# Kernel tuning notes

Measured on AMD Instinct MI355X. Metric: run time of the kernel, lower is better.

## Reference

```python
import jax, jax.numpy as jnp
import numpy as np
from jax import lax

N, D, M, H = 8192, 32, 8, 128
ATOL = 1e-5
RTOL = 1e-5
MAX_STEPS = 10   # bounded adaptive dopri5 iterations (accept/reject with masking)
DT0 = 0.25


def setup_inputs() -> dict:
    key = jax.random.key(0)
    ks = jax.random.split(key, 6)
    p = lambda k, shape, s: jax.random.normal(k, shape, jnp.float32) * s
    return {
        "z": jax.random.normal(ks[0], (N, D), jnp.float32),
        "G_w": p(ks[1], (M, D), 0.3),
        "W1": p(ks[2], (H, D), (1.0 / D) ** 0.5),
        "b1": jnp.zeros((H,), jnp.float32),
        "W2": p(ks[3], (H, H), (1.0 / H) ** 0.5),
        "b2": jnp.zeros((H,), jnp.float32),
        "W3": p(ks[4], (D, H), (1.0 / H) ** 0.5),
        "b3": jnp.zeros((D,), jnp.float32),
        "T": jnp.ones((1,), jnp.float32),
    }


def qpnf_forward(z, G_w, W1, b1, W2, b2, W3, b3, T):
    d = z.shape[1]

    def mlp(x):  # dF network: d -> 128 -> 128 -> d
        h = jax.nn.relu(x @ W1.T + b1)
        h = jax.nn.relu(h @ W2.T + b2)
        return h @ W3.T + b3

    # G is linear (no bias) so jacrev(G)(x) == G_w for every sample; the batched
    # dG @ dG^T solves collapse to one shared (m,m) solve / (d,d) projector.
    A = G_w @ G_w.T                       # (m, m)
    AinvG = jnp.linalg.solve(A, G_w)      # (m, d) = A^{-1} W
    P = G_w.T @ AinvG                     # (d, d) null-space projector W^T A^{-1} W
    IP = jnp.eye(d, dtype=z.dtype) - P
    trP = jnp.trace(P)

    jac_mlp = jax.vmap(jax.jacrev(lambda xi: mlp(xi[None, :])[0]))  # (N,d,d)

    def f(y):  # augmented state y = [x | logp], dlogp/dt = -div(dx/dx)
        x = y[:, :d]
        dF = mlp(x)                        # (N, d)
        g = x @ G_w.T                      # (N, m)
        dz = -(dF @ IP) - g @ AinvG        # -(eta_J) - (eta_C)
        JdF = jac_mlp(x)                   # (N, d, d)
        # J_f = -(I-P) JdF - P  ->  dlogp = -trace(J_f)
        dlogp = jnp.einsum('jk,nkj->n', IP, JdF) + trP
        return jnp.concatenate([dz, dlogp[:, None]], axis=1)

    def rk_step(y, dt):  # Dormand-Prince 5(4)
        k1 = f(y)
        k2 = f(y + dt * (0.2 * k1))
        k3 = f(y + dt * (3/40 * k1 + 9/40 * k2))
        k4 = f(y + dt * (44/45 * k1 - 56/15 * k2 + 32/9 * k3))
        k5 = f(y + dt * (19372/6561 * k1 - 25360/2187 * k2 + 64448/6561 * k3 - 212/729 * k4))
        k6 = f(y + dt * (9017/3168 * k1 - 355/33 * k2 + 46732/5247 * k3 + 49/176 * k4 - 5103/18656 * k5))
        y1 = y + dt * (35/384 * k1 + 500/1113 * k3 + 125/192 * k4 - 2187/6784 * k5 + 11/84 * k6)
        k7 = f(y1)
        err = dt * ((35/384 - 5179/57600) * k1 + (500/1113 - 7571/16695) * k3
                    + (125/192 - 393/640) * k4 + (-2187/6784 + 92097/339200) * k5
                    + (11/84 - 187/2100) * k6 - (1/40) * k7)
        return y1, err

    t1 = 2.0 * T[0]  # eval path: integration_times[-1] *= 2
    y0 = jnp.concatenate([z, jnp.zeros((z.shape[0], 1), z.dtype)], axis=1)

    def body(carry, _):
        t, dt, y = carry
        done = t >= t1 - 1e-9
        dtc = jnp.where(done, jnp.asarray(1e-3, z.dtype), jnp.minimum(dt, t1 - t))
        y1, ev = rk_step(y, dtc)
        tol = ATOL + RTOL * jnp.maximum(jnp.abs(y), jnp.abs(y1))
        errn = jnp.sqrt(jnp.mean((ev / tol) ** 2))
        accept = jnp.logical_and(~done, errn <= 1.0)
        y_new = jnp.where(accept, y1, y)
        t_new = jnp.where(accept, t + dtc, t)
        factor = jnp.clip(0.9 * errn ** (-0.2), 0.2, 10.0)
        dt_new = jnp.where(done, dt, jnp.clip(dtc * factor, 1e-6, t1))
        dt_new = lax.stop_gradient(dt_new)
        return (t_new, dt_new, y_new), None

    init = (jnp.asarray(0.0, z.dtype), jnp.asarray(DT0, z.dtype), y0)
    (_, _, yT), _ = lax.scan(body, init, None, length=MAX_STEPS)
    return yT[:, :d]


def reference(z, G_w, W1, b1, W2, b2, W3, b3, T):
    return qpnf_forward(z, G_w, W1, b1, W2, b2, W3, b3, T)
```

## Files before the change

### kernel.cpp

```cpp
#include <hip/hip_runtime.h>
#include <hip/hip_cooperative_groups.h>
#include <math.h>

namespace cg = cooperative_groups;
typedef float4 f4;

#define NT 512
#define RB 32

#define WS_WR    0
#define WS_PART  32768
#define WS_TOTAL 35328

#define L_W1T   0
#define L_C3T   4096
#define L_P     8320
#define L_PT    9344
#define L_HST   10496
#define L_HS2   15104
#define L_XST   19712
#define L_B1    20864
#define L_B2    20992
#define L_C0    21120
#define L_GS    21152
#define L_AAUG  21408
#define L_AINVG 21536
#define L_MISC  21792
#define L_KZ    21796
#define L_KL    29860
#define L_YZ    30084
#define L_Y1Z   31236
#define L_YL    32388
#define L_Y1L   32420
#define LDS_FLOATS 32452
#define L_RED   L_XST

__device__ const float ACO[5][5] = {
  { 0.2f, 0.f, 0.f, 0.f, 0.f },
  { (float)(3.0/40.0), (float)(9.0/40.0), 0.f, 0.f, 0.f },
  { (float)(44.0/45.0), (float)(-56.0/15.0), (float)(32.0/9.0), 0.f, 0.f },
  { (float)(19372.0/6561.0), (float)(-25360.0/2187.0), (float)(64448.0/6561.0), (float)(-212.0/729.0), 0.f },
  { (float)(9017.0/3168.0), (float)(-355.0/33.0), (float)(46732.0/5247.0), (float)(49.0/176.0), (float)(-5103.0/18656.0) }
};

#define B1C ((float)(35.0/384.0))
#define B3C ((float)(500.0/1113.0))
#define B4C ((float)(125.0/192.0))
#define B5C ((float)(-2187.0/6784.0))
#define B6C ((float)(11.0/84.0))

#define E1C ((float)(35.0/384.0 - 5179.0/57600.0))
#define E3C ((float)(500.0/1113.0 - 7571.0/16695.0))
#define E4C ((float)(125.0/192.0 - 393.0/640.0))
#define E5C ((float)(-2187.0/6784.0 + 92097.0/339200.0))
#define E6C ((float)(11.0/84.0 - 187.0/2100.0))
#define E7C ((float)(-1.0/40.0))

__device__ __forceinline__ f4 ld4(const float* p){ return *(const f4*)p; }
__device__ __forceinline__ void st4(float* p, f4 v){ *(f4*)p = v; }

__device__ void assemble_x(float* lds, int tid, float dtc, const float* co, int np)
{
  __syncthreads();
  if (tid < 256){
    const int r = tid >> 3, jj = (tid & 7) * 4;
    const int o = r * 36 + jj;
    f4 y = ld4(&lds[L_YZ + o]);
    float sx = 0.f, sy = 0.f, sz = 0.f, sw = 0.f;
    for (int p = 0; p < np; p++){
      f4 kv = ld4(&lds[L_KZ + p * 1152 + o]);
      float c = co[p];
      sx += c * kv.x; sy += c * kv.y; sz += c * kv.z; sw += c * kv.w;
    }
    lds[L_XST + (jj + 0) * 36 + r] = y.x + dtc * sx;
    lds[L_XST + (jj + 1) * 36 + r] = y.y + dtc * sy;
    lds[L_XST + (jj + 2) * 36 + r] = y.z + dtc * sz;
    lds[L_XST + (jj + 3) * 36 + r] = y.w + dtc * sw;
  }
  __syncthreads();
}

__device__ void eval_f(float* lds, const float* __restrict__ ws, int tid,
                       float trP, int kout)
{
  const int cg = tid & 31, kh = (tid >> 5) & 1, wv = tid >> 6;
  const int row4 = 4 * wv;

  float a1[4][4];
#pragma unroll
  for (int i = 0; i < 4; i++)
#pragma unroll
    for (int j = 0; j < 4; j++) a1[i][j] = 0.f;
#pragma unroll 4
  for (int t = 0; t < 16; t++){
    const int k = kh * 16 + t;
    f4 av = ld4(&lds[L_XST + k * 36 + row4]);
    f4 bv = ld4(&lds[L_W1T + k * 128 + 4 * cg]);
    const float* ap = (const float*)&av;
    const float* bp = (const float*)&bv;
#pragma unroll
    for (int i = 0; i < 4; i++)
#pragma unroll
      for (int j = 0; j < 4; j++) a1[i][j] += bp[i] * ap[j];
  }
#pragma unroll
  for (int i = 0; i < 4; i++)
#pragma unroll
    for (int j = 0; j < 4; j++) a1[i][j] += __shfl_xor(a1[i][j], 32);
  if (kh == 0){
    f4 b1v = ld4(&lds[L_B1 + 4 * cg]);
    const float* b1p = (const float*)&b1v;
#pragma unroll
    for (int i = 0; i < 4; i++){
      f4 hv; float* hp = (float*)&hv;
#pragma unroll
      for (int j = 0; j < 4; j++) hp[j] = fmaxf(a1[i][j] + b1p[i], 0.f);
      st4(&lds[L_HST + (4 * cg + i) * 36 + row4], hv);
    }
  }
  __syncthreads();

  float ah[4][4], at[4][4];
#pragma unroll
  for (int i = 0; i < 4; i++)
#pragma unroll
    for (int j = 0; j < 4; j++){ ah[i][j] = 0.f; at[i][j] = 0.f; }
  const f4* WR4 = (const f4*)&ws[WS_WR];
  const int kb = kh * 64;
  f4 wb[4], rb[4];
#pragma unroll
  for (int u = 0; u < 4; u++){
    wb[u] = WR4[(kb + u) * 64 + cg];
    rb[u] = WR4[(kb + u) * 64 + 32 + cg];
  }
#pragma unroll 1
  for (int g = 0; g < 16; g++){
    f4 wc[4], rc[4];
#pragma unroll
    for (int u = 0; u < 4; u++){ wc[u] = wb[u]; rc[u] = rb[u]; }
    if (g < 15){
      const int kn = kb + (g + 1) * 4;
#pragma unroll
      for (int u = 0; u < 4; u++){
        wb[u] = WR4[(kn + u) * 64 + cg];
        rb[u] = WR4[(kn + u) * 64 + 32 + cg];
      }
    }
#pragma unroll
    for (int u = 0; u < 4; u++){
      const int k = kb + g * 4 + u;
      f4 av = ld4(&lds[L_HST + k * 36 + row4]);
      const float* ap = (const float*)&av;
      const float* wp = (const float*)&wc[u];
      const float* rp = (const float*)&rc[u];
      float m[4];
#pragma unroll
      for (int j = 0; j < 4; j++) m[j] = (ap[j] > 0.f) ? 1.f : 0.f;
#pragma unroll
      for (int i = 0; i < 4; i++)
#pragma unroll
        for (int j = 0; j < 4; j++){
          ah[i][j] += wp[i] * ap[j];
          at[i][j] += rp[i] * m[j];
        }
    }
  }
#pragma unroll
  for (int i = 0; i < 4; i++)
#pragma unroll
    for (int j = 0; j < 4; j++){
      ah[i][j] += __shfl_xor(ah[i][j], 32);
      at[i][j] += __shfl_xor(at[i][j], 32);
    }

  f4 b2v = ld4(&lds[L_B2 + 4 * cg]);
  const float* b2p = (const float*)&b2v;
  float h2v[4][4]; float dl[4] = {0.f, 0.f, 0.f, 0.f};
#pragma unroll
  for (int i = 0; i < 4; i++)
#pragma unroll
    for (int j = 0; j < 4; j++){
      float pre = ah[i][j] + b2p[i];
      float hv = fmaxf(pre, 0.f);
      h2v[i][j] = hv;
      if (pre > 0.f) dl[j] += at[i][j];
    }
#pragma unroll
  for (int mk = 1; mk < 32; mk <<= 1){
#pragma unroll
    for (int j = 0; j < 4; j++) dl[j] += __shfl_xor(dl[j], mk, 64);
  }
  if (kh == 0){
#pragma unroll
    for (int i = 0; i < 4; i++){
      f4 hv; float* hp = (float*)&hv;
#pragma unroll
      for (int j = 0; j < 4; j++) hp[j] = h2v[i][j];
      st4(&lds[L_HS2 + (4 * cg + i) * 36 + row4], hv);
    }
    if (cg == 0){
#pragma unroll
      for (int j = 0; j < 4; j++)
        lds[L_KL + kout * 32 + row4 + j] = dl[j] + trP;
    }
  }
  __syncthreads();

  float a3[4] = {0.f, 0.f, 0.f, 0.f};
  const int bb = kh * 64;
#pragma unroll 4
  for (int t = 0; t < 16; t++){
    f4 cv = ld4(&lds[L_C3T + cg * 132 + bb + 4 * t]);
    const float* cp = (const float*)&cv;
#pragma unroll
    for (int u = 0; u < 4; u++){
      f4 av = ld4(&lds[L_HS2 + (bb + 4 * t + u) * 36 + row4]);
      const float* ap = (const float*)&av;
#pragma unroll
      for (int j = 0; j < 4; j++) a3[j] += ap[j] * cp[u];
    }
  }
  const int qq = kh * 16;
#pragma unroll
  for (int t = 0; t < 4; t++){
    f4 pv = ld4(&lds[L_PT + cg * 36 + qq + 4 * t]);
    const float* pp = (const float*)&pv;
#pragma unroll
    for (int u = 0; u < 4; u++){
      f4 av = ld4(&lds[L_XST + (qq + 4 * t + u) * 36 + row4]);
      const float* ap = (const float*)&av;
#pragma unroll
      for (int j = 0; j < 4; j++) a3[j] += ap[j] * pp[u];
    }
  }
#pragma unroll
  for (int j = 0; j < 4; j++) a3[j] += __shfl_xor(a3[j], 32);
  if (kh == 0){
    float c0v = lds[L_C0 + cg];
#pragma unroll
    for (int j = 0; j < 4; j++)
      lds[L_KZ + kout * 1152 + (row4 + j) * 36 + cg] = -(a3[j] + c0v);
  }
}

__global__ void __launch_bounds__(NT, 2)
qpnf_kernel(const float* __restrict__ z, const float* __restrict__ Gw,
            const float* __restrict__ W1g, const float* __restrict__ b1g,
            const float* __restrict__ W2g, const float* __restrict__ b2g,
            const float* __restrict__ W3g, const float* __restrict__ b3g,
            const float* __restrict__ Tg, float* __restrict__ out,
            float* __restrict__ ws)
{
  __shared__ float lds[LDS_FLOATS];
  const int tid = threadIdx.x;
  const int bid = blockIdx.x;
  const int r0 = bid * RB;
  cg::grid_group grid = cg::this_grid();

  for (int i = 0; i < 8; i++){
    int idx = tid + i * NT;
    int h = idx >> 5, j = idx & 31;
    lds[L_W1T + j * 128 + h] = W1g[idx];
  }
  if (tid < 128){ lds[L_B1 + tid] = b1g[tid]; lds[L_B2 + tid] = b2g[tid]; }
  if (tid < 256) lds[L_GS + tid] = Gw[tid];
  __syncthreads();

  if (tid < 64){
    int i = tid >> 3, j = tid & 7;
    float s = 0.f;
    for (int k = 0; k < 32; k++) s += lds[L_GS + i * 32 + k] * lds[L_GS + j * 32 + k];
    lds[L_AAUG + i * 16 + j] = s;
    lds[L_AAUG + i * 16 + 8 + j] = (i == j) ? 1.f : 0.f;
  }
  __syncthreads();
  if (tid == 0){
    float* A = &lds[L_AAUG];
    for (int c = 0; c < 8; c++){
      int p = c; float mx = fabsf(A[c * 16 + c]);
      for (int r = c + 1; r < 8; r++){
        float v = fabsf(A[r * 16 + c]);
        if (v > mx){ mx = v; p = r; }
      }
      if (p != c)
        for (int q = 0; q < 16; q++){ float t = A[c*16+q]; A[c*16+q] = A[p*16+q]; A[p*16+q] = t; }
      float pv = 1.0f / A[c * 16 + c];
      for (int q = 0; q < 16; q++) A[c * 16 + q] *= pv;
      for (int r = 0; r < 8; r++) if (r != c){
        float fct = A[r * 16 + c];
        for (int q = 0; q < 16; q++) A[r * 16 + q] -= fct * A[c * 16 + q];
      }
    }
  }
  __syncthreads();
  if (tid < 256){
    int m = tid >> 5, d = tid & 31;
    float s = 0.f;
    for (int q = 0; q < 8; q++) s += lds[L_AAUG + m * 16 + 8 + q] * lds[L_GS + q * 32 + d];
    lds[L_AINVG + m * 32 + d] = s;
  }
  __syncthreads();
  for (int i4 = 0; i4 < 2; i4++){
    int idx = tid + i4 * NT;
    int i = idx >> 5, j = idx & 31;
    float s = 0.f;
    for (int m = 0; m < 8; m++) s += lds[L_GS + m * 32 + i] * lds[L_AINVG + m * 32 + j];
    lds[L_P + i * 32 + j] = s;
  }
  __syncthreads();
  float* IPl = &lds[L_XST];
  for (int i4 = 0; i4 < 2; i4++){
    int idx = tid + i4 * NT;
    int i = idx >> 5, j = idx & 31;
    IPl[i * 32 + j] = ((i == j) ? 1.f : 0.f) - lds[L_P + i * 32 + j];
  }
  if (tid == 0){
    float s = 0.f;
    for (int i = 0; i < 32; i++) s += lds[L_P + i * 32 + i];
    lds[L_MISC] = s;
  }
  __syncthreads();
  for (int i4 = 0; i4 < 8; i4++){
    int idx = tid + i4 * NT;
    int b = idx & 127, c = idx >> 7;
    float s = 0.f;
    for (int i = 0; i < 32; i++) s += W3g[i * 128 + b] * IPl[i * 32 + c];
    lds[L_C3T + c * 132 + b] = s;
  }
  for (int i4 = 0; i4 < 2; i4++){
    int idx = tid + i4 * NT;
    int c = idx >> 5, q = idx & 31;
    lds[L_PT + c * 36 + q] = lds[L_P + q * 32 + c];
  }
  if (tid < 32){
    float s = 0.f;
    for (int i = 0; i < 32; i++) s += b3g[i] * IPl[i * 32 + tid];
    lds[L_C0 + tid] = s;
  }
  for (int i4 = 0; i4 < 8; i4++){
    int idx = tid + i4 * NT;
    int j = idx >> 7, b = idx & 127;
    float s = 0.f;
    for (int k = 0; k < 32; k++) s += IPl[j * 32 + k] * W3g[k * 128 + b];
    lds[L_HST + j * 128 + b] = s;
  }
  __syncthreads();
  if (bid < 128 && tid < 128){
    int a = bid;
    float s = 0.f;
    for (int j = 0; j < 32; j++) s += W1g[a * 32 + j] * lds[L_HST + j * 128 + tid];
    ws[WS_WR + a * 256 + 128 + tid] = s * W2g[tid * 128 + a];
  }
  if (bid >= 128 && tid < 128){
    int a = bid - 128;
    ws[WS_WR + a * 256 + tid] = W2g[tid * 128 + a];
  }
  if (tid < 256){
    const int r = tid >> 3, jj = (tid & 7) * 4;
    st4(&lds[L_YZ + r * 36 + jj], ld4(&z[(r0 + r) * 32 + jj]));
  }
  if (tid < RB) lds[L_YL + tid] = 0.f;

  const float trP = lds[L_MISC];
  const float t1 = 2.0f * Tg[0];

  grid.sync();

  float t_cur = 0.f, dt_cur = 0.25f;
  bool prev_acc = false;

  for (int step = 0; step < 10; step++){
    if (t_cur >= t1 - 1e-9f) break;
    const float dtc = fminf(dt_cur, t1 - t_cur);

    for (int s = 1; s <= 6; s++){
      if (s == 1 && step > 0){
        if (prev_acc){
          if (tid < 256){
            const int r = tid >> 3, jj = (tid & 7) * 4;
            const int o = r * 36 + jj;
            st4(&lds[L_KZ + o], ld4(&lds[L_KZ + 6 * 1152 + o]));
          }
          if (tid < RB) lds[L_KL + tid] = lds[L_KL + 6 * 32 + tid];
        }
        continue;
      }
      assemble_x(lds, tid, dtc, ACO[s >= 2 ? s - 2 : 0], s - 1);
      eval_f(lds, ws, tid, trP, s - 1);
    }

    __syncthreads();
    if (tid < 256){
      const int r = tid >> 3, jj = (tid & 7) * 4;
      const int o = r * 36 + jj;
      f4 y   = ld4(&lds[L_YZ + o]);
      f4 k1v = ld4(&lds[L_KZ + 0 * 1152 + o]);
      f4 k3v = ld4(&lds[L_KZ + 2 * 1152 + o]);
      f4 k4v = ld4(&lds[L_KZ + 3 * 1152 + o]);
      f4 k5v = ld4(&lds[L_KZ + 4 * 1152 + o]);
      f4 k6v = ld4(&lds[L_KZ + 5 * 1152 + o]);
      f4 x;
      x.x = y.x + dtc * (B1C*k1v.x + B3C*k3v.x + B4C*k4v.x + B5C*k5v.x + B6C*k6v.x);
      x.y = y.y + dtc * (B1C*k1v.y + B3C*k3v.y + B4C*k4v.y + B5C*k5v.y + B6C*k6v.y);
      x.z = y.z + dtc * (B1C*k1v.z + B3C*k3v.z + B4C*k4v.z + B5C*k5v.z + B6C*k6v.z);
      x.w = y.w + dtc * (B1C*k1v.w + B3C*k3v.w + B4C*k4v.w + B5C*k5v.w + B6C*k6v.w);
      st4(&lds[L_Y1Z + o], x);
      lds[L_XST + (jj + 0) * 36 + r] = x.x;
      lds[L_XST + (jj + 1) * 36 + r] = x.y;
      lds[L_XST + (jj + 2) * 36 + r] = x.z;
      lds[L_XST + (jj + 3) * 36 + r] = x.w;
    }
    if (tid < RB){
      float s = B1C * lds[L_KL + 0*32 + tid] + B3C * lds[L_KL + 2*32 + tid]
              + B4C * lds[L_KL + 3*32 + tid] + B5C * lds[L_KL + 4*32 + tid]
              + B6C * lds[L_KL + 5*32 + tid];
      lds[L_Y1L + tid] = lds[L_YL + tid] + dtc * s;
    }
    __syncthreads();
    eval_f(lds, ws, tid, trP, 6);
    __syncthreads();

    float sacc = 0.f;
    if (tid < 256){
      const int r = tid >> 3, jj = (tid & 7) * 4;
      const int o = r * 36 + jj;
      f4 k1v = ld4(&lds[L_KZ + 0 * 1152 + o]);
      f4 k3v = ld4(&lds[L_KZ + 2 * 1152 + o]);
      f4 k4v = ld4(&lds[L_KZ + 3 * 1152 + o]);
      f4 k5v = ld4(&lds[L_KZ + 4 * 1152 + o]);
      f4 k6v = ld4(&lds[L_KZ + 5 * 1152 + o]);
      f4 k7v = ld4(&lds[L_KZ + 6 * 1152 + o]);
      f4 yv  = ld4(&lds[L_YZ + o]);
      f4 y1v = ld4(&lds[L_Y1Z + o]);
      float ev, tol, q;
      ev = dtc * (E1C*k1v.x + E3C*k3v.x + E4C*k4v.x + E5C*k5v.x + E6C*k6v.x + E7C*k7v.x);
      tol = 1e-5f + 1e-5f * fmaxf(fabsf(yv.x), fabsf(y1v.x)); q = ev / tol; sacc += q * q;
      ev = dtc * (E1C*k1v.y + E3C*k3v.y + E4C*k4v.y + E5C*k5v.y + E6C*k6v.y + E7C*k7v.y);
      tol = 1e-5f + 1e-5f * fmaxf(fabsf(yv.y), fabsf(y1v.y)); q = ev / tol; sacc += q * q;
      ev = dtc * (E1C*k1v.z + E3C*k3v.z + E4C*k4v.z + E5C*k5v.z + E6C*k6v.z + E7C*k7v.z);
      tol = 1e-5f + 1e-5f * fmaxf(fabsf(yv.z), fabsf(y1v.z)); q = ev / tol; sacc += q * q;
      ev = dtc * (E1C*k1v.w + E3C*k3v.w + E4C*k4v.w + E5C*k5v.w + E6C*k6v.w + E7C*k7v.w);
      tol = 1e-5f + 1e-5f * fmaxf(fabsf(yv.w), fabsf(y1v.w)); q = ev / tol; sacc += q * q;
    }
    if (tid < RB){
      float evl = dtc * (E1C * lds[L_KL + 0*32 + tid] + E3C * lds[L_KL + 2*32 + tid]
                + E4C * lds[L_KL + 3*32 + tid] + E5C * lds[L_KL + 4*32 + tid]
                + E6C * lds[L_KL + 5*32 + tid] + E7C * lds[L_KL + 6*32 + tid]);
      float toll = 1e-5f + 1e-5f * fmaxf(fabsf(lds[L_YL + tid]), fabsf(lds[L_Y1L + tid]));
      float ql = evl / toll; sacc += ql * ql;
    }
    __syncthreads();
    lds[L_RED + tid] = sacc; __syncthreads();
    for (int o = 256; o > 0; o >>= 1){
      if (tid < o) lds[L_RED + tid] += lds[L_RED + tid + o];
      __syncthreads();
    }
    if (tid == 0) ws[WS_PART + step * 256 + bid] = lds[L_RED + 0];

    grid.sync();

    if (tid < 256) lds[L_RED + tid] = ws[WS_PART + step * 256 + tid];
    __syncthreads();
    for (int o = 128; o > 0; o >>= 1){
      if (tid < o) lds[L_RED + tid] += lds[L_RED + tid + o];
      __syncthreads();
    }
    const float errn = sqrtf(lds[L_RED + 0] / 270336.0f);
    __syncthreads();

    const bool accept = (errn <= 1.0f);
    if (accept){
      if (tid < 256){
        const int r = tid >> 3, jj = (tid & 7) * 4;
        const int o = r * 36 + jj;
        st4(&lds[L_YZ + o], ld4(&lds[L_Y1Z + o]));
      }
      if (tid < RB) lds[L_YL + tid] = lds[L_Y1L + tid];
      t_cur += dtc;
    }
    float fac = 0.9f * powf(errn, -0.2f);
    fac = fminf(fmaxf(fac, 0.2f), 10.0f);
    dt_cur = fminf(fmaxf(dtc * fac, 1e-6f), t1);
    prev_acc = accept;
  }

  __syncthreads();
  if (tid < 256){
    const int r = tid >> 3, jj = (tid & 7) * 4;
    st4(&out[(r0 + r) * 32 + jj], ld4(&lds[L_YZ + r * 36 + jj]));
  }
}

extern "C" void kernel_launch(void* const* d_in, const int* in_sizes, int n_in,
                              void* d_out, int out_size, void* d_ws, size_t ws_size,
                              hipStream_t stream)
{
  (void)in_sizes; (void)n_in; (void)out_size;
  const float* z  = (const float*)d_in[0];
  const float* Gw = (const float*)d_in[1];
  const float* W1 = (const float*)d_in[2];
  const float* b1 = (const float*)d_in[3];
  const float* W2 = (const float*)d_in[4];
  const float* b2 = (const float*)d_in[5];
  const float* W3 = (const float*)d_in[6];
  const float* b3 = (const float*)d_in[7];
  const float* T  = (const float*)d_in[8];
  float* out = (float*)d_out;
  float* ws  = (float*)d_ws;
  if (ws_size < (size_t)WS_TOTAL * sizeof(float)) return;

  void* args[] = { (void*)&z, (void*)&Gw, (void*)&W1, (void*)&b1, (void*)&W2,
                   (void*)&b2, (void*)&W3, (void*)&b3, (void*)&T, (void*)&out,
                   (void*)&ws };
  hipLaunchCooperativeKernel((const void*)qpnf_kernel, dim3(256), dim3(NT),
                             args, 0, stream);
}
```

Before: 1.300 ms.

## Give each wave its own rows so RK stage evaluation avoids block barriers

Each wave now owns 4 rows of the block's 32-row tile and runs the MLP stage evaluation on private per-wave LDS buffers with swizzled layouts. This replaces the block-wide __syncthreads between stages with wave-local fences, and the final error reduction uses wave shuffles instead of a shared-memory tree. The cost is that each wave now reads all of W2/W3 (global WR loads and LDS C3T) for only 4 rows, which raises weight traffic per row. Correctness relies on wave-lockstep execution with only __threadfence_block for ordering.

```diff
diff --git a/kernel.cpp b/kernel.cpp
--- a/kernel.cpp
+++ b/kernel.cpp
@@ -4,6 +4,7 @@
 
 namespace cg = cooperative_groups;
 typedef float4 f4;
+typedef float2 f2;
 
 #define NT 512
 #define RB 32
@@ -13,27 +14,31 @@
 #define WS_TOTAL 35328
 
 #define L_W1T   0
-#define L_C3T   4096
-#define L_P     8320
-#define L_PT    9344
-#define L_HST   10496
-#define L_HS2   15104
-#define L_XST   19712
-#define L_B1    20864
-#define L_B2    20992
-#define L_C0    21120
-#define L_GS    21152
-#define L_AAUG  21408
-#define L_AINVG 21536
-#define L_MISC  21792
-#define L_KZ    21796
-#define L_KL    29860
-#define L_YZ    30084
-#define L_Y1Z   31236
-#define L_YL    32388
-#define L_Y1L   32420
-#define LDS_FLOATS 32452
-#define L_RED   L_XST
+#define L_C3T   4240
+#define L_PT    8976
+#define L_KZ    10384
+#define L_KL    18448
+#define L_YZ    18672
+#define L_Y1Z   19824
+#define L_YL    20976
+#define L_Y1L   21008
+#define L_B1    21040
+#define L_B2    21168
+#define L_C0    21296
+#define L_MISC  21328
+#define L_RED8  21332
+#define L_WV    21340
+#define WVSZ    1200
+#define WV_XW   0
+#define WV_HW   140
+#define WV_H2   668
+#define LDS_FLOATS 30940
+
+#define LI_GS    (L_WV + 0)
+#define LI_AAUG  (L_WV + 256)
+#define LI_AINVG (L_WV + 384)
+#define LI_P     (L_WV + 640)
+#define LI_IPW3  (L_WV + 1664)
 
 __device__ const float ACO[5][5] = {
   { 0.2f, 0.f, 0.f, 0.f, 0.f },
@@ -59,188 +64,235 @@
 __device__ __forceinline__ f4 ld4(const float* p){ return *(const f4*)p; }
 __device__ __forceinline__ void st4(float* p, f4 v){ *(f4*)p = v; }
 
-__device__ void assemble_x(float* lds, int tid, float dtc, const float* co, int np)
+__device__ void assemble_wave(float* lds, int lane, int w, float dtc,
+                              const float* co, int np)
 {
-  __syncthreads();
-  if (tid < 256){
-    const int r = tid >> 3, jj = (tid & 7) * 4;
-    const int o = r * 36 + jj;
-    f4 y = ld4(&lds[L_YZ + o]);
-    float sx = 0.f, sy = 0.f, sz = 0.f, sw = 0.f;
-    for (int p = 0; p < np; p++){
-      f4 kv = ld4(&lds[L_KZ + p * 1152 + o]);
-      float c = co[p];
-      sx += c * kv.x; sy += c * kv.y; sz += c * kv.z; sw += c * kv.w;
-    }
-    lds[L_XST + (jj + 0) * 36 + r] = y.x + dtc * sx;
-    lds[L_XST + (jj + 1) * 36 + r] = y.y + dtc * sy;
-    lds[L_XST + (jj + 2) * 36 + r] = y.z + dtc * sz;
-    lds[L_XST + (jj + 3) * 36 + r] = y.w + dtc * sw;
-  }
-  __syncthreads();
+  const int row = lane >> 4, c0 = 2 * (lane & 15);
+  const int yo = (4 * w + row) * 36 + c0;
+  f2 y = *(const f2*)&lds[L_YZ + yo];
+  float sx = 0.f, sy = 0.f;
+  for (int p = 0; p < np; p++){
+    f2 kv = *(const f2*)&lds[L_KZ + p * 1152 + yo];
+    sx += co[p] * kv.x; sy += co[p] * kv.y;
+  }
+  float* XW = &lds[L_WV + w * WVSZ + WV_XW];
+  const int s0 = 4 * c0 + 4 * ((c0 >> 3) & 3);
+  XW[s0 + row]     = y.x + dtc * sx;
+  XW[s0 + 4 + row] = y.y + dtc * sy;
+  __threadfence_block();
 }
 
-__device__ void eval_f(float* lds, const float* __restrict__ ws, int tid,
-                       float trP, int kout)
+__device__ void eval_wave(float* lds, const float* __restrict__ ws,
+                          int lane, int w, float trP, int kout)
 {
-  const int cg = tid & 31, kh = (tid >> 5) & 1, wv = tid >> 6;
-  const int row4 = 4 * wv;
-
-  float a1[4][4];
-#pragma unroll
-  for (int i = 0; i < 4; i++)
+  const int cg = lane & 15, kh = lane >> 4;
+  float* XW = &lds[L_WV + w * WVSZ + WV_XW];
+  float* HW = &lds[L_WV + w * WVSZ + WV_HW];
+  float* H2 = &lds[L_WV + w * WVSZ + WV_H2];
+
+  float a1[8][4];
+#pragma unroll
+  for (int i = 0; i < 8; i++)
 #pragma unroll
     for (int j = 0; j < 4; j++) a1[i][j] = 0.f;
-#pragma unroll 4
-  for (int t = 0; t < 16; t++){
-    const int k = kh * 16 + t;
-    f4 av = ld4(&lds[L_XST + k * 36 + row4]);
-    f4 bv = ld4(&lds[L_W1T + k * 128 + 4 * cg]);
+#pragma unroll
+  for (int t = 0; t < 8; t++){
+    const int k = kh * 8 + t;
+    f4 av = ld4(&XW[4 * k + 4 * kh]);
+    f4 b0 = ld4(&lds[L_W1T + k * 132 + 4 * kh + 8 * cg]);
+    f4 b1v = ld4(&lds[L_W1T + k * 132 + 4 * kh + 8 * cg + 4]);
     const float* ap = (const float*)&av;
-    const float* bp = (const float*)&bv;
+    const float* bp0 = (const float*)&b0;
+    const float* bp1 = (const float*)&b1v;
 #pragma unroll
     for (int i = 0; i < 4; i++)
 #pragma unroll
-      for (int j = 0; j < 4; j++) a1[i][j] += bp[i] * ap[j];
-  }
-#pragma unroll
-  for (int i = 0; i < 4; i++)
-#pragma unroll
-    for (int j = 0; j < 4; j++) a1[i][j] += __shfl_xor(a1[i][j], 32);
+      for (int j = 0; j < 4; j++){
+        a1[i][j]     += bp0[i] * ap[j];
+        a1[4 + i][j] += bp1[i] * ap[j];
+      }
+  }
+#pragma unroll
+  for (int i = 0; i < 8; i++)
+#pragma unroll
+    for (int j = 0; j < 4; j++){
+      a1[i][j] += __shfl_xor(a1[i][j], 16);
+      a1[i][j] += __shfl_xor(a1[i][j], 32);
+    }
   if (kh == 0){
-    f4 b1v = ld4(&lds[L_B1 + 4 * cg]);
-    const float* b1p = (const float*)&b1v;
-#pragma unroll
-    for (int i = 0; i < 4; i++){
+    f4 bb0 = ld4(&lds[L_B1 + 8 * cg]);
+    f4 bb1 = ld4(&lds[L_B1 + 8 * cg + 4]);
+    const float* bp0 = (const float*)&bb0;
+    const float* bp1 = (const float*)&bb1;
+    const int swz = 4 * ((cg >> 2) & 3);
+#pragma unroll
+    for (int i = 0; i < 8; i++){
+      float bi = (i < 4) ? bp0[i] : bp1[i - 4];
       f4 hv; float* hp = (float*)&hv;
 #pragma unroll
-      for (int j = 0; j < 4; j++) hp[j] = fmaxf(a1[i][j] + b1p[i], 0.f);
-      st4(&lds[L_HST + (4 * cg + i) * 36 + row4], hv);
-    }
-  }
-  __syncthreads();
-
-  float ah[4][4], at[4][4];
-#pragma unroll
-  for (int i = 0; i < 4; i++)
+      for (int j = 0; j < 4; j++) hp[j] = fmaxf(a1[i][j] + bi, 0.f);
+      st4(&HW[4 * (8 * cg + i) + swz], hv);
+    }
+  }
+  __threadfence_block();
+
+  float ah[8][4], at[8][4];
+#pragma unroll
+  for (int i = 0; i < 8; i++)
 #pragma unroll
     for (int j = 0; j < 4; j++){ ah[i][j] = 0.f; at[i][j] = 0.f; }
   const f4* WR4 = (const f4*)&ws[WS_WR];
-  const int kb = kh * 64;
-  f4 wb[4], rb[4];
-#pragma unroll
-  for (int u = 0; u < 4; u++){
-    wb[u] = WR4[(kb + u) * 64 + cg];
-    rb[u] = WR4[(kb + u) * 64 + 32 + cg];
+  const int kb = kh * 32;
+  f4 buf[8];
+#pragma unroll
+  for (int e = 0; e < 2; e++){
+    buf[4*e+0] = WR4[(kb + e) * 64 + 2 * cg];
+    buf[4*e+1] = WR4[(kb + e) * 64 + 2 * cg + 1];
+    buf[4*e+2] = WR4[(kb + e) * 64 + 32 + 2 * cg];
+    buf[4*e+3] = WR4[(kb + e) * 64 + 32 + 2 * cg + 1];
   }
 #pragma unroll 1
   for (int g = 0; g < 16; g++){
-    f4 wc[4], rc[4];
-#pragma unroll
-    for (int u = 0; u < 4; u++){ wc[u] = wb[u]; rc[u] = rb[u]; }
+    f4 cur[8];
+#pragma unroll
+    for (int u = 0; u < 8; u++) cur[u] = buf[u];
     if (g < 15){
-      const int kn = kb + (g + 1) * 4;
-#pragma unroll
-      for (int u = 0; u < 4; u++){
-        wb[u] = WR4[(kn + u) * 64 + cg];
-        rb[u] = WR4[(kn + u) * 64 + 32 + cg];
-      }
-    }
+      const int kn = kb + 2 * (g + 1);
+#pragma unroll
+      for (int e = 0; e < 2; e++){
+        buf[4*e+0] = WR4[(kn + e) * 64 + 2 * cg];
+        buf[4*e+1] = WR4[(kn + e) * 64 + 2 * cg + 1];
+        buf[4*e+2] = WR4[(kn + e) * 64 + 32 + 2 * cg];
+        buf[4*e+3] = WR4[(kn + e) * 64 + 32 + 2 * cg + 1];
+      }
+    }
+#pragma unroll
+    for (int e = 0; e < 2; e++){
+      const int k = kb + 2 * g + e;
+      f4 av = ld4(&HW[4 * k + 4 * kh]);
+      const float* ap = (const float*)&av;
+      const float* wa = (const float*)&cur[4*e+0];
+      const float* wb = (const float*)&cur[4*e+1];
+      const float* ra = (const float*)&cur[4*e+2];
+      const float* rb = (const float*)&cur[4*e+3];
+      float m[4];
+#pragma unroll
+      for (int j = 0; j < 4; j++) m[j] = (ap[j] > 0.f) ? 1.f : 0.f;
+#pragma unroll
+      for (int i = 0; i < 4; i++)
+#pragma unroll
+        for (int j = 0; j < 4; j++){
+          ah[i][j]     += wa[i] * ap[j];
+          ah[4 + i][j] += wb[i] * ap[j];
+          at[i][j]     += ra[i] * m[j];
+          at[4 + i][j] += rb[i] * m[j];
+        }
+    }
+  }
+#pragma unroll
+  for (int i = 0; i < 8; i++)
+#pragma unroll
+    for (int j = 0; j < 4; j++){
+      ah[i][j] += __shfl_xor(ah[i][j], 16);
+      ah[i][j] += __shfl_xor(ah[i][j], 32);
+      at[i][j] += __shfl_xor(at[i][j], 16);
+      at[i][j] += __shfl_xor(at[i][j], 32);
+    }
+
+  f4 b2a = ld4(&lds[L_B2 + 8 * cg]);
+  f4 b2b = ld4(&lds[L_B2 + 8 * cg + 4]);
+  const float* b2p0 = (const float*)&b2a;
+  const float* b2p1 = (const float*)&b2b;
+  float h2v[8][4]; float dl[4] = {0.f, 0.f, 0.f, 0.f};
+#pragma unroll
+  for (int i = 0; i < 8; i++){
+    float bi = (i < 4) ? b2p0[i] : b2p1[i - 4];
+#pragma unroll
+    for (int j = 0; j < 4; j++){
+      float pre = ah[i][j] + bi;
+      h2v[i][j] = fmaxf(pre, 0.f);
+      if (pre > 0.f) dl[j] += at[i][j];
+    }
+  }
+#pragma unroll
+  for (int mk = 1; mk < 16; mk <<= 1){
+#pragma unroll
+    for (int j = 0; j < 4; j++) dl[j] += __shfl_xor(dl[j], mk);
+  }
+  if (lane == 0){
+#pragma unroll
+    for (int j = 0; j < 4; j++)
+      lds[L_KL + kout * 32 + 4 * w + j] = dl[j] + trP;
+  }
+  if (kh == 0){
+    const int swz = 4 * ((cg >> 2) & 3);
+#pragma unroll
+    for (int i = 0; i < 8; i++){
+      f4 hv; float* hp = (float*)&hv;
+#pragma unroll
+      for (int j = 0; j < 4; j++) hp[j] = h2v[i][j];
+      st4(&H2[4 * (8 * cg + i) + swz], hv);
+    }
+  }
+  __threadfence_block();
+
+  float a3[2][4] = {{0.f,0.f,0.f,0.f},{0.f,0.f,0.f,0.f}};
+  const int cc0 = 2 * cg, cc1 = 2 * cg + 1;
+  const int bb = kh * 32;
+#pragma unroll 2
+  for (int t = 0; t < 8; t++){
+    const int b4 = bb + 4 * t;
+    f4 cva = ld4(&lds[L_C3T + cc0 * 148 + b4 + 4 * kh]);
+    f4 cvb = ld4(&lds[L_C3T + cc1 * 148 + b4 + 4 * kh]);
+    const float* ca = (const float*)&cva;
+    const float* cb = (const float*)&cvb;
 #pragma unroll
     for (int u = 0; u < 4; u++){
-      const int k = kb + g * 4 + u;
-      f4 av = ld4(&lds[L_HST + k * 36 + row4]);
+      f4 av = ld4(&H2[4 * (b4 + u) + 4 * kh]);
       const float* ap = (const float*)&av;
-      const float* wp = (const float*)&wc[u];
-      const float* rp = (const float*)&rc[u];
-      float m[4];
-#pragma unroll
-      for (int j = 0; j < 4; j++) m[j] = (ap[j] > 0.f) ? 1.f : 0.f;
-#pragma unroll
-      for (int i = 0; i < 4; i++)
-#pragma unroll
-        for (int j = 0; j < 4; j++){
-          ah[i][j] += wp[i] * ap[j];
-          at[i][j] += rp[i] * m[j];
-        }
-    }
-  }
-#pragma unroll
-  for (int i = 0; i < 4; i++)
+#pragma unroll
+      for (int j = 0; j < 4; j++){
+        a3[0][j] += ap[j] * ca[u];
+        a3[1][j] += ap[j] * cb[u];
+      }
+    }
+  }
+  const int qq = kh * 8;
+#pragma unroll
+  for (int t = 0; t < 2; t++){
+    const int q4 = qq + 4 * t;
+    f4 pva = ld4(&lds[L_PT + cc0 * 44 + q4 + 4 * kh]);
+    f4 pvb = ld4(&lds[L_PT + cc1 * 44 + q4 + 4 * kh]);
+    const float* pa = (const float*)&pva;
+    const float* pb = (const float*)&pvb;
+#pragma unroll
+    for (int u = 0; u < 4; u++){
+      f4 av = ld4(&XW[4 * (q4 + u) + 4 * kh]);
+      const float* ap = (const float*)&av;
+#pragma unroll
+      for (int j = 0; j < 4; j++){
+        a3[0][j] += ap[j] * pa[u];
+        a3[1][j] += ap[j] * pb[u];
+      }
+    }
+  }
+#pragma unroll
+  for (int j = 0; j < 4; j++){
+    a3[0][j] += __shfl_xor(a3[0][j], 16);
+    a3[0][j] += __shfl_xor(a3[0][j], 32);
+    a3[1][j] += __shfl_xor(a3[1][j], 16);
+    a3[1][j] += __shfl_xor(a3[1][j], 32);
+  }
+  if (kh == 0){
+    float c0v = lds[L_C0 + cc0];
+    float c1v = lds[L_C0 + cc1];
 #pragma unroll
     for (int j = 0; j < 4; j++){
-      ah[i][j] += __shfl_xor(ah[i][j], 32);
-      at[i][j] += __shfl_xor(at[i][j], 32);
-    }
-
-  f4 b2v = ld4(&lds[L_B2 + 4 * cg]);
-  const float* b2p = (const float*)&b2v;
-  float h2v[4][4]; float dl[4] = {0.f, 0.f, 0.f, 0.f};
-#pragma unroll
-  for (int i = 0; i < 4; i++)
-#pragma unroll
-    for (int j = 0; j < 4; j++){
-      float pre = ah[i][j] + b2p[i];
-      float hv = fmaxf(pre, 0.f);
-      h2v[i][j] = hv;
-      if (pre > 0.f) dl[j] += at[i][j];
-    }
-#pragma unroll
-  for (int mk = 1; mk < 32; mk <<= 1){
-#pragma unroll
-    for (int j = 0; j < 4; j++) dl[j] += __shfl_xor(dl[j], mk, 64);
-  }
-  if (kh == 0){
-#pragma unroll
-    for (int i = 0; i < 4; i++){
-      f4 hv; float* hp = (float*)&hv;
-#pragma unroll
-      for (int j = 0; j < 4; j++) hp[j] = h2v[i][j];
-      st4(&lds[L_HS2 + (4 * cg + i) * 36 + row4], hv);
-    }
-    if (cg == 0){
-#pragma unroll
-      for (int j = 0; j < 4; j++)
-        lds[L_KL + kout * 32 + row4 + j] = dl[j] + trP;
-    }
-  }
-  __syncthreads();
-
-  float a3[4] = {0.f, 0.f, 0.f, 0.f};
-  const int bb = kh * 64;
-#pragma unroll 4
-  for (int t = 0; t < 16; t++){
-    f4 cv = ld4(&lds[L_C3T + cg * 132 + bb + 4 * t]);
-    const float* cp = (const float*)&cv;
-#pragma unroll
-    for (int u = 0; u < 4; u++){
-      f4 av = ld4(&lds[L_HS2 + (bb + 4 * t + u) * 36 + row4]);
-      const float* ap = (const float*)&av;
-#pragma unroll
-      for (int j = 0; j < 4; j++) a3[j] += ap[j] * cp[u];
-    }
-  }
-  const int qq = kh * 16;
-#pragma unroll
-  for (int t = 0; t < 4; t++){
-    f4 pv = ld4(&lds[L_PT + cg * 36 + qq + 4 * t]);
-    const float* pp = (const float*)&pv;
-#pragma unroll
-    for (int u = 0; u < 4; u++){
-      f4 av = ld4(&lds[L_XST + (qq + 4 * t + u) * 36 + row4]);
-      const float* ap = (const float*)&av;
-#pragma unroll
-      for (int j = 0; j < 4; j++) a3[j] += ap[j] * pp[u];
-    }
-  }
-#pragma unroll
-  for (int j = 0; j < 4; j++) a3[j] += __shfl_xor(a3[j], 32);
-  if (kh == 0){
-    float c0v = lds[L_C0 + cg];
-#pragma unroll
-    for (int j = 0; j < 4; j++)
-      lds[L_KZ + kout * 1152 + (row4 + j) * 36 + cg] = -(a3[j] + c0v);
-  }
+      f2 kv; kv.x = -(a3[0][j] + c0v); kv.y = -(a3[1][j] + c1v);
+      *(f2*)&lds[L_KZ + kout * 1152 + (4 * w + j) * 36 + cc0] = kv;
+    }
+  }
+  __threadfence_block();
 }
 
 __global__ void __launch_bounds__(NT, 2)
@@ -255,27 +307,23 @@
   const int tid = threadIdx.x;
   const int bid = blockIdx.x;
   const int r0 = bid * RB;
+  const int lane = tid & 63, w = tid >> 6;
   cg::grid_group grid = cg::this_grid();
 
-  for (int i = 0; i < 8; i++){
-    int idx = tid + i * NT;
-    int h = idx >> 5, j = idx & 31;
-    lds[L_W1T + j * 128 + h] = W1g[idx];
-  }
   if (tid < 128){ lds[L_B1 + tid] = b1g[tid]; lds[L_B2 + tid] = b2g[tid]; }
-  if (tid < 256) lds[L_GS + tid] = Gw[tid];
+  if (tid < 256) lds[LI_GS + tid] = Gw[tid];
   __syncthreads();
 
   if (tid < 64){
     int i = tid >> 3, j = tid & 7;
     float s = 0.f;
-    for (int k = 0; k < 32; k++) s += lds[L_GS + i * 32 + k] * lds[L_GS + j * 32 + k];
-    lds[L_AAUG + i * 16 + j] = s;
-    lds[L_AAUG + i * 16 + 8 + j] = (i == j) ? 1.f : 0.f;
+    for (int k = 0; k < 32; k++) s += lds[LI_GS + i * 32 + k] * lds[LI_GS + j * 32 + k];
+    lds[LI_AAUG + i * 16 + j] = s;
+    lds[LI_AAUG + i * 16 + 8 + j] = (i == j) ? 1.f : 0.f;
   }
   __syncthreads();
   if (tid == 0){
-    float* A = &lds[L_AAUG];
+    float* A = &lds[LI_AAUG];
     for (int c = 0; c < 8; c++){
       int p = c; float mx = fabsf(A[c * 16 + c]);
       for (int r = c + 1; r < 8; r++){
@@ -296,59 +344,64 @@
   if (tid < 256){
     int m = tid >> 5, d = tid & 31;
     float s = 0.f;
-    for (int q = 0; q < 8; q++) s += lds[L_AAUG + m * 16 + 8 + q] * lds[L_GS + q * 32 + d];
-    lds[L_AINVG + m * 32 + d] = s;
-  }
-  __syncthreads();
-  for (int i4 = 0; i4 < 2; i4++){
-    int idx = tid + i4 * NT;
+    for (int q = 0; q < 8; q++) s += lds[LI_AAUG + m * 16 + 8 + q] * lds[LI_GS + q * 32 + d];
+    lds[LI_AINVG + m * 32 + d] = s;
+  }
+  __syncthreads();
+  for (int i2 = 0; i2 < 2; i2++){
+    int idx = tid + i2 * NT;
+    int q = idx >> 5, c = idx & 31;
+    float s = 0.f;
+    for (int m = 0; m < 8; m++) s += lds[LI_GS + m * 32 + q] * lds[LI_AINVG + m * 32 + c];
+    lds[LI_P + q * 32 + c] = s;
+  }
+  __syncthreads();
+  for (int i2 = 0; i2 < 2; i2++){
+    int idx = tid + i2 * NT;
+    int c = idx >> 5, q = idx & 31;
+    lds[L_PT + c * 44 + q + 4 * ((q >> 3) & 3)] = lds[LI_P + q * 32 + c];
+  }
+  if (tid == 0){
+    float s = 0.f;
+    for (int i = 0; i < 32; i++) s += lds[LI_P + i * 32 + i];
+    lds[L_MISC] = s;
+  }
+  __syncthreads();
+  for (int i2 = 0; i2 < 2; i2++){
+    int idx = tid + i2 * NT;
     int i = idx >> 5, j = idx & 31;
-    float s = 0.f;
-    for (int m = 0; m < 8; m++) s += lds[L_GS + m * 32 + i] * lds[L_AINVG + m * 32 + j];
-    lds[L_P + i * 32 + j] = s;
-  }
-  __syncthreads();
-  float* IPl = &lds[L_XST];
-  for (int i4 = 0; i4 < 2; i4++){
-    int idx = tid + i4 * NT;
-    int i = idx >> 5, j = idx & 31;
-    IPl[i * 32 + j] = ((i == j) ? 1.f : 0.f) - lds[L_P + i * 32 + j];
-  }
-  if (tid == 0){
-    float s = 0.f;
-    for (int i = 0; i < 32; i++) s += lds[L_P + i * 32 + i];
-    lds[L_MISC] = s;
-  }
-  __syncthreads();
-  for (int i4 = 0; i4 < 8; i4++){
-    int idx = tid + i4 * NT;
-    int b = idx & 127, c = idx >> 7;
-    float s = 0.f;
-    for (int i = 0; i < 32; i++) s += W3g[i * 128 + b] * IPl[i * 32 + c];
-    lds[L_C3T + c * 132 + b] = s;
-  }
-  for (int i4 = 0; i4 < 2; i4++){
-    int idx = tid + i4 * NT;
-    int c = idx >> 5, q = idx & 31;
-    lds[L_PT + c * 36 + q] = lds[L_P + q * 32 + c];
+    lds[LI_P + i * 32 + j] = ((i == j) ? 1.f : 0.f) - lds[LI_P + i * 32 + j];
+  }
+  __syncthreads();
+  for (int i8 = 0; i8 < 8; i8++){
+    int idx = tid + i8 * NT;
+    int c = idx >> 7, b = idx & 127;
+    float s = 0.f;
+    for (int i = 0; i < 32; i++) s += W3g[i * 128 + b] * lds[LI_P + i * 32 + c];
+    lds[L_C3T + c * 148 + b + 4 * ((b >> 5) & 3)] = s;
   }
   if (tid < 32){
     float s = 0.f;
-    for (int i = 0; i < 32; i++) s += b3g[i] * IPl[i * 32 + tid];
+    for (int i = 0; i < 32; i++) s += b3g[i] * lds[LI_P + i * 32 + tid];
     lds[L_C0 + tid] = s;
   }
-  for (int i4 = 0; i4 < 8; i4++){
-    int idx = tid + i4 * NT;
+  for (int i8 = 0; i8 < 8; i8++){
+    int idx = tid + i8 * NT;
     int j = idx >> 7, b = idx & 127;
     float s = 0.f;
-    for (int k = 0; k < 32; k++) s += IPl[j * 32 + k] * W3g[k * 128 + b];
-    lds[L_HST + j * 128 + b] = s;
+    for (int k = 0; k < 32; k++) s += lds[LI_P + j * 32 + k] * W3g[k * 128 + b];
+    lds[LI_IPW3 + j * 128 + b] = s;
+  }
+  for (int i8 = 0; i8 < 8; i8++){
+    int idx = tid + i8 * NT;
+    int h = idx >> 5, j = idx & 31;
+    lds[L_W1T + j * 132 + 4 * ((j >> 3) & 3) + h] = W1g[idx];
   }
   __syncthreads();
   if (bid < 128 && tid < 128){
     int a = bid;
     float s = 0.f;
-    for (int j = 0; j < 32; j++) s += W1g[a * 32 + j] * lds[L_HST + j * 128 + tid];
+    for (int j = 0; j < 32; j++) s += W1g[a * 32 + j] * lds[LI_IPW3 + j * 128 + tid];
     ws[WS_WR + a * 256 + 128 + tid] = s * W2g[tid * 128 + a];
   }
   if (bid >= 128 && tid < 128){
@@ -361,6 +414,7 @@
   }
   if (tid < RB) lds[L_YL + tid] = 0.f;
 
+  __syncthreads();
   const float trP = lds[L_MISC];
   const float t1 = 2.0f * Tg[0];
 
@@ -373,107 +427,102 @@
     if (t_cur >= t1 - 1e-9f) break;
     const float dtc = fminf(dt_cur, t1 - t_cur);
 
-    for (int s = 1; s <= 6; s++){
-      if (s == 1 && step > 0){
-        if (prev_acc){
-          if (tid < 256){
-            const int r = tid >> 3, jj = (tid & 7) * 4;
-            const int o = r * 36 + jj;
-            st4(&lds[L_KZ + o], ld4(&lds[L_KZ + 6 * 1152 + o]));
-          }
-          if (tid < RB) lds[L_KL + tid] = lds[L_KL + 6 * 32 + tid];
-        }
-        continue;
-      }
-      assemble_x(lds, tid, dtc, ACO[s >= 2 ? s - 2 : 0], s - 1);
-      eval_f(lds, ws, tid, trP, s - 1);
-    }
-
-    __syncthreads();
-    if (tid < 256){
-      const int r = tid >> 3, jj = (tid & 7) * 4;
-      const int o = r * 36 + jj;
-      f4 y   = ld4(&lds[L_YZ + o]);
-      f4 k1v = ld4(&lds[L_KZ + 0 * 1152 + o]);
-      f4 k3v = ld4(&lds[L_KZ + 2 * 1152 + o]);
-      f4 k4v = ld4(&lds[L_KZ + 3 * 1152 + o]);
-      f4 k5v = ld4(&lds[L_KZ + 4 * 1152 + o]);
-      f4 k6v = ld4(&lds[L_KZ + 5 * 1152 + o]);
-      f4 x;
+    if (step == 0){
+      assemble_wave(lds, lane, w, dtc, ACO[0], 0);
+      eval_wave(lds, ws, lane, w, trP, 0);
+    } else if (prev_acc){
+      const int row = lane >> 4, c0 = 2 * (lane & 15);
+      const int yo = (4 * w + row) * 36 + c0;
+      *(f2*)&lds[L_KZ + yo] = *(const f2*)&lds[L_KZ + 6 * 1152 + yo];
+      if (lane < 4) lds[L_KL + 4 * w + lane] = lds[L_KL + 6 * 32 + 4 * w + lane];
+      __threadfence_block();
+    }
+
+    for (int s = 2; s <= 6; s++){
+      assemble_wave(lds, lane, w, dtc, ACO[s - 2], s - 1);
+      eval_wave(lds, ws, lane, w, trP, s - 1);
+    }
+
+    {
+      const int row = lane >> 4, c0 = 2 * (lane & 15);
+      const int yo = (4 * w + row) * 36 + c0;
+      f2 y   = *(const f2*)&lds[L_YZ + yo];
+      f2 k1v = *(const f2*)&lds[L_KZ + 0 * 1152 + yo];
+      f2 k3v = *(const f2*)&lds[L_KZ + 2 * 1152 + yo];
+      f2 k4v = *(const f2*)&lds[L_KZ + 3 * 1152 + yo];
+      f2 k5v = *(const f2*)&lds[L_KZ + 4 * 1152 + yo];
+      f2 k6v = *(const f2*)&lds[L_KZ + 5 * 1152 + yo];
+      f2 x;
       x.x = y.x + dtc * (B1C*k1v.x + B3C*k3v.x + B4C*k4v.x + B5C*k5v.x + B6C*k6v.x);
       x.y = y.y + dtc * (B1C*k1v.y + B3C*k3v.y + B4C*k4v.y + B5C*k5v.y + B6C*k6v.y);
-      x.z = y.z + dtc * (B1C*k1v.z + B3C*k3v.z + B4C*k4v.z + B5C*k5v.z + B6C*k6v.z);
-      x.w = y.w + dtc * (B1C*k1v.w + B3C*k3v.w + B4C*k4v.w + B5C*k5v.w + B6C*k6v.w);
-      st4(&lds[L_Y1Z + o], x);
-      lds[L_XST + (jj + 0) * 36 + r] = x.x;
-      lds[L_XST + (jj + 1) * 36 + r] = x.y;
-      lds[L_XST + (jj + 2) * 36 + r] = x.z;
-      lds[L_XST + (jj + 3) * 36 + r] = x.w;
-    }
-    if (tid < RB){
-      float s = B1C * lds[L_KL + 0*32 + tid] + B3C * lds[L_KL + 2*32 + tid]
-              + B4C * lds[L_KL + 3*32 + tid] + B5C * lds[L_KL + 4*32 + tid]
-              + B6C * lds[L_KL + 5*32 + tid];
-      lds[L_Y1L + tid] = lds[L_YL + tid] + dtc * s;
-    }
-    __syncthreads();
-    eval_f(lds, ws, tid, trP, 6);
-    __syncthreads();
+      *(f2*)&lds[L_Y1Z + yo] = x;
+      float* XW = &lds[L_WV + w * WVSZ + WV_XW];
+      const int s0 = 4 * c0 + 4 * ((c0 >> 3) & 3);
+      XW[s0 + row]     = x.x;
+      XW[s0 + 4 + row] = x.y;
+      if (lane < 4){
+        int n = 4 * w + lane;
+        float s = B1C * lds[L_KL + 0*32 + n] + B3C * lds[L_KL + 2*32 + n]
+                + B4C * lds[L_KL + 3*32 + n] + B5C * lds[L_KL + 4*32 + n]
+                + B6C * lds[L_KL + 5*32 + n];
+        lds[L_Y1L + n] = lds[L_YL + n] + dtc * s;
+      }
+      __threadfence_block();
+    }
+    eval_wave(lds, ws, lane, w, trP, 6);
 
     float sacc = 0.f;
-    if (tid < 256){
-      const int r = tid >> 3, jj = (tid & 7) * 4;
-      const int o = r * 36 + jj;
-      f4 k1v = ld4(&lds[L_KZ + 0 * 1152 + o]);
-      f4 k3v = ld4(&lds[L_KZ + 2 * 1152 + o]);
-      f4 k4v = ld4(&lds[L_KZ + 3 * 1152 + o]);
-      f4 k5v = ld4(&lds[L_KZ + 4 * 1152 + o]);
-      f4 k6v = ld4(&lds[L_KZ + 5 * 1152 + o]);
-      f4 k7v = ld4(&lds[L_KZ + 6 * 1152 + o]);
-      f4 yv  = ld4(&lds[L_YZ + o]);
-      f4 y1v = ld4(&lds[L_Y1Z + o]);
+    {
+      const int row = lane >> 4, c0 = 2 * (lane & 15);
+      const int yo = (4 * w + row) * 36 + c0;
+      f2 k1v = *(const f2*)&lds[L_KZ + 0 * 1152 + yo];
+      f2 k3v = *(const f2*)&lds[L_KZ + 2 * 1152 + yo];
+      f2 k4v = *(const f2*)&lds[L_KZ + 3 * 1152 + yo];
+      f2 k5v = *(const f2*)&lds[L_KZ + 4 * 1152 + yo];
+      f2 k6v = *(const f2*)&lds[L_KZ + 5 * 1152 + yo];
+      f2 k7v = *(const f2*)&lds[L_KZ + 6 * 1152 + yo];
+      f2 yv  = *(const f2*)&lds[L_YZ + yo];
+      f2 y1v = *(const f2*)&lds[L_Y1Z + yo];
       float ev, tol, q;
       ev = dtc * (E1C*k1v.x + E3C*k3v.x + E4C*k4v.x + E5C*k5v.x + E6C*k6v.x + E7C*k7v.x);
       tol = 1e-5f + 1e-5f * fmaxf(fabsf(yv.x), fabsf(y1v.x)); q = ev / tol; sacc += q * q;
       ev = dtc * (E1C*k1v.y + E3C*k3v.y + E4C*k4v.y + E5C*k5v.y + E6C*k6v.y + E7C*k7v.y);
       tol = 1e-5f + 1e-5f * fmaxf(fabsf(yv.y), fabsf(y1v.y)); q = ev / tol; sacc += q * q;
-      ev = dtc * (E1C*k1v.z + E3C*k3v.z + E4C*k4v.z + E5C*k5v.z + E6C*k6v.z + E7C*k7v.z);
-      tol = 1e-5f + 1e-5f * fmaxf(fabsf(yv.z), fabsf(y1v.z)); q = ev / tol; sacc += q * q;
-      ev = dtc * (E1C*k1v.w + E3C*k3v.w + E4C*k4v.w + E5C*k5v.w + E6C*k6v.w + E7C*k7v.w);
-      tol = 1e-5f + 1e-5f * fmaxf(fabsf(yv.w), fabsf(y1v.w)); q = ev / tol; sacc += q * q;
-    }
-    if (tid < RB){
-      float evl = dtc * (E1C * lds[L_KL + 0*32 + tid] + E3C * lds[L_KL + 2*32 + tid]
-                + E4C * lds[L_KL + 3*32 + tid] + E5C * lds[L_KL + 4*32 + tid]
-                + E6C * lds[L_KL + 5*32 + tid] + E7C * lds[L_KL + 6*32 + tid]);
-      float toll = 1e-5f + 1e-5f * fmaxf(fabsf(lds[L_YL + tid]), fabsf(lds[L_Y1L + tid]));
-      float ql = evl / toll; sacc += ql * ql;
-    }
+      if (lane < 4){
+        int n = 4 * w + lane;
+        float evl = dtc * (E1C * lds[L_KL + 0*32 + n] + E3C * lds[L_KL + 2*32 + n]
+                  + E4C * lds[L_KL + 3*32 + n] + E5C * lds[L_KL + 4*32 + n]
+                  + E6C * lds[L_KL + 5*32 + n] + E7C * lds[L_KL + 6*32 + n]);
+        float toll = 1e-5f + 1e-5f * fmaxf(fabsf(lds[L_YL + n]), fabsf(lds[L_Y1L + n]));
+        float ql = evl / toll; sacc += ql * ql;
+      }
+    }
+#pragma unroll
+    for (int mk = 1; mk < 64; mk <<= 1) sacc += __shfl_xor(sacc, mk);
+    if (lane == 0) lds[L_RED8 + w] = sacc;
     __syncthreads();
-    lds[L_RED + tid] = sacc; __syncthreads();
-    for (int o = 256; o > 0; o >>= 1){
-      if (tid < o) lds[L_RED + tid] += lds[L_RED + tid + o];
-      __syncthreads();
-    }
-    if (tid == 0) ws[WS_PART + step * 256 + bid] = lds[L_RED + 0];
-
+    if (tid == 0){
+      float s = 0.f;
+      for (int i = 0; i < 8; i++) s += lds[L_RED8 + i];
+      ws[WS_PART + step * 256 + bid] = s;
+    }
     grid.sync();
 
-    if (tid < 256) lds[L_RED + tid] = ws[WS_PART + step * 256 + tid];
+    float* red = &lds[L_WV];
+    if (tid < 256) red[tid] = ws[WS_PART + step * 256 + tid];
     __syncthreads();
     for (int o = 128; o > 0; o >>= 1){
-      if (tid < o) lds[L_RED + tid] += lds[L_RED + tid + o];
+      if (tid < o) red[tid] += red[tid + o];
       __syncthreads();
     }
-    const float errn = sqrtf(lds[L_RED + 0] / 270336.0f);
+    const float errn = sqrtf(red[0] / 270336.0f);
     __syncthreads();
 
     const bool accept = (errn <= 1.0f);
     if (accept){
       if (tid < 256){
         const int r = tid >> 3, jj = (tid & 7) * 4;
-        const int o = r * 36 + jj;
-        st4(&lds[L_YZ + o], ld4(&lds[L_Y1Z + o]));
+        st4(&lds[L_YZ + r * 36 + jj], ld4(&lds[L_Y1Z + r * 36 + jj]));
       }
       if (tid < RB) lds[L_YL + tid] = lds[L_Y1L + tid];
       t_cur += dtc;
@@ -482,6 +531,7 @@
     fac = fminf(fmaxf(fac, 0.2f), 10.0f);
     dt_cur = fminf(fmaxf(dtc * fac, 1e-6f), t1);
     prev_acc = accept;
+    __syncthreads();
   }
 
   __syncthreads();
```

Result: slower. 1.366 ms (+5.1%).
